# Performance work log

Hardware: AMD Instinct MI355X
Metric: run time of the kernel (lower is better)

## Reference

```python
import jax, jax.numpy as jnp
import numpy as np

EPS = 1e-8  # torch.nn.CosineSimilarity default eps


def setup_inputs() -> dict:
    key = jax.random.key(0)
    ks = jax.random.split(key, 7)
    B, T, D = 2048, 128, 128
    x = jax.random.normal(ks[0], (B, T, D), dtype=jnp.float32)
    def lin(k, fan_out, fan_in):
        kw, kb = jax.random.split(k)
        bound = 1.0 / np.sqrt(fan_in)
        W = jax.random.uniform(kw, (fan_out, fan_in), minval=-bound, maxval=bound, dtype=jnp.float32)
        b = jax.random.uniform(kb, (fan_out,), minval=-bound, maxval=bound, dtype=jnp.float32)
        return W, b
    W1, b1 = lin(ks[1], 96, 128)
    W2, b2 = lin(ks[2], 72, 96)
    W3, b3 = lin(ks[3], 64, 72)
    return {"x": x, "W1": W1, "b1": b1, "W2": W2, "b2": b2, "W3": W3, "b3": b3}


def reference(x, W1, b1, W2, b2, W3, b3):
    # Batched 3-layer MLP (equivalent to the per-slice Python loop).
    h = jax.nn.relu(jnp.einsum('btd,od->bto', x, W1) + b1)
    h = jax.nn.relu(jnp.einsum('bth,oh->bto', h, W2) + b2)
    f = jnp.einsum('bth,oh->bto', h, W3) + b3          # [B, T, 64]
    f = f.reshape(-1, f.shape[-1])                      # [N, 64], N = B*T
    n = jnp.maximum(jnp.linalg.norm(f, axis=-1, keepdims=True), EPS)
    u = f / n                                           # row-normalized feats
    # sum_{i<j} u_i . u_j = (||sum_i u_i||^2 - sum_i ||u_i||^2) / 2
    s = u.sum(axis=0)                                   # [64]
    pair_sum = 0.5 * (jnp.dot(s, s) - jnp.sum(u * u))
    return pair_sum / f.shape[0]
```

## Files before the change

### kernel.cpp

```cpp
#include <hip/hip_runtime.h>

typedef float  f32x4  __attribute__((ext_vector_type(4)));
typedef short  s16x8  __attribute__((ext_vector_type(8)));
typedef short  s16x4  __attribute__((ext_vector_type(4)));

#define NROWS (2048 * 128)
#define PASSES 8
#define HS 104
#define EPSF 1e-8f

union Frag { s16x8 v; unsigned short u[8]; };

__device__ __forceinline__ unsigned short f2bf(float f) {
    unsigned int u = __float_as_uint(f);
    u += 0x7fffu + ((u >> 16) & 1u);
    return (unsigned short)(u >> 16);
}

__global__ void repack(const float* __restrict__ W1, const float* __restrict__ b1,
                       const float* __restrict__ W2, const float* __restrict__ b2,
                       const float* __restrict__ W3, const float* __restrict__ b3,
                       unsigned short* __restrict__ w1f, unsigned short* __restrict__ w2f,
                       unsigned short* __restrict__ w3f,
                       float* __restrict__ b1p, float* __restrict__ b2p,
                       float* __restrict__ b3p)
{
    const int b = blockIdx.x;
    const int l = threadIdx.x;
    const int g = l >> 4, sl = l & 15;

    if (b < 24) {
        const int nt = b >> 2, ks = b & 3;
        const int o = nt * 16 + sl, kb = ks * 32 + g * 8;
        s16x8 v;
#pragma unroll
        for (int j = 0; j < 8; ++j) v[j] = (short)f2bf(W1[o * 128 + kb + j]);
        *(s16x8*)&w1f[b * 512 + l * 8] = v;
    } else if (b < 39) {
        const int f = b - 24, nt = f / 3, ks = f % 3;
        const int o = nt * 16 + sl, kb = ks * 32 + g * 8;
        s16x8 v;
#pragma unroll
        for (int j = 0; j < 8; ++j)
            v[j] = (short)((o < 72) ? f2bf(W2[o * 96 + kb + j]) : 0);
        *(s16x8*)&w2f[f * 512 + l * 8] = v;
    } else if (b < 51) {
        const int f = b - 39, nt = f / 3, ks = f % 3;
        const int o = nt * 16 + sl, kb = ks * 32 + g * 8;
        s16x8 v;
#pragma unroll
        for (int j = 0; j < 8; ++j)
            v[j] = (short)((kb + j < 72) ? f2bf(W3[o * 72 + kb + j]) : 0);
        *(s16x8*)&w3f[f * 512 + l * 8] = v;
    } else {
        for (int i = l; i < 240; i += 64) {
            if (i < 96)       b1p[i] = b1[i];
            else if (i < 176) { int o = i - 96; b2p[o] = (o < 72) ? b2[o] : 0.f; }
            else              b3p[i - 176] = b3[i - 176];
        }
    }
}

__global__ __launch_bounds__(256, 1)
void mlp_main(const float* __restrict__ x,
              const f32x4* __restrict__ w1src,
              const unsigned short* __restrict__ w2f,
              const unsigned short* __restrict__ w3f,
              float* __restrict__ acc )
{
    __shared__ __align__(16) unsigned char  wb[25536];
    __shared__ __align__(16) float          xbuf[4][2048];
    __shared__ __align__(16) unsigned short act[4][16][HS];
    __shared__ float sred[4][64];
    __shared__ float uured[4];

    const unsigned short* w1L = (const unsigned short*)wb;
    const float* b1L = (const float*)(wb + 24576);
    const float* b2L = b1L + 96;
    const float* b3L = b1L + 176;

    const int tid  = threadIdx.x;
    const int lane = tid & 63;
    const int wv   = tid >> 6;
    const int g    = lane >> 4;
    const int sl   = lane & 15;
    const int g4   = g * 4;
    const int wave_gid = blockIdx.x * 4 + wv;

    auto stage = [&](int p) {
        const char* tb = (const char*)x
                       + ((size_t)wave_gid * 128 + (size_t)p * 16) * 512;
        float* dst = &xbuf[wv][0];
#pragma unroll
        for (int c = 0; c < 8; ++c) {
            const unsigned off = (unsigned)(c * 1024 + lane * 16);
            const unsigned so  = off ^ (((off >> 9) & 7u) << 4);
            __builtin_amdgcn_global_load_lds(
                (const __attribute__((address_space(1))) void*)(tb + so),
                (__attribute__((address_space(3))) void*)(dst + c * 256),
                16, 0, 0);
        }
    };

    stage(0);

    for (int i = tid; i < 1596; i += 256)
        ((f32x4*)wb)[i] = w1src[i];

    Frag W2r[5][3], W3r[4][3];
#pragma unroll
    for (int nt = 0; nt < 5; ++nt)
#pragma unroll
        for (int ks = 0; ks < 3; ++ks)
            W2r[nt][ks].v = *(const s16x8*)&w2f[(nt * 3 + ks) * 512 + lane * 8];
#pragma unroll
    for (int nt = 0; nt < 4; ++nt)
#pragma unroll
        for (int ks = 0; ks < 3; ++ks)
            W3r[nt][ks].v = *(const s16x8*)&w3f[(nt * 3 + ks) * 512 + lane * 8];

    __syncthreads();

    float uu_part = 0.f;
    float s_part[4][4];
#pragma unroll
    for (int nt = 0; nt < 4; ++nt)
#pragma unroll
        for (int r = 0; r < 4; ++r) s_part[nt][r] = 0.f;

#pragma unroll 1
    for (int p = 0; p < PASSES; ++p) {
        asm volatile("s_waitcnt vmcnt(0)" ::: "memory");
        __builtin_amdgcn_sched_barrier(0);

        const char* xb = (const char*)&xbuf[wv][0];
        const unsigned sw = (unsigned)((sl & 7) << 4);
        f32x4 t[8];
#pragma unroll
        for (int ks = 0; ks < 4; ++ks)
#pragma unroll
            for (int h = 0; h < 2; ++h)
                t[ks * 2 + h] = *(const f32x4*)(
                    xb + sl * 512 + ks * 128 + (((unsigned)(g * 32 + h * 16)) ^ sw));
        Frag X1[4];
#pragma unroll
        for (int ks = 0; ks < 4; ++ks)
#pragma unroll
            for (int j = 0; j < 4; ++j) {
                X1[ks].u[j]     = f2bf(t[ks * 2 + 0][j]);
                X1[ks].u[4 + j] = f2bf(t[ks * 2 + 1][j]);
            }

        __builtin_amdgcn_sched_barrier(0);
        if (p + 1 < PASSES) stage(p + 1);

        f32x4 D1[6];
#pragma unroll
        for (int nt = 0; nt < 6; ++nt)
            D1[nt] = *(const f32x4*)&b1L[nt * 16 + g4];
#pragma unroll
        for (int ks = 0; ks < 4; ++ks)
#pragma unroll
            for (int nt = 0; nt < 6; ++nt) {
                const s16x8 Wf = *(const s16x8*)&w1L[(nt * 4 + ks) * 512 + lane * 8];
                D1[nt] = __builtin_amdgcn_mfma_f32_16x16x32_bf16(Wf, X1[ks].v, D1[nt], 0, 0, 0);
            }
#pragma unroll
        for (int nt = 0; nt < 6; ++nt) {
            s16x4 q;
#pragma unroll
            for (int j = 0; j < 4; ++j) q[j] = (short)f2bf(fmaxf(D1[nt][j], 0.f));
            *(s16x4*)&act[wv][sl][nt * 16 + g4] = q;
        }

        Frag A2[3];
#pragma unroll
        for (int ks = 0; ks < 3; ++ks)
            A2[ks].v = *(const s16x8*)&act[wv][sl][ks * 32 + g * 8];

        {
            const s16x4 z = (s16x4){0, 0, 0, 0};
            *(s16x4*)&act[wv][sl][80 + g4] = z;
        }

        f32x4 D2[5];
#pragma unroll
        for (int nt = 0; nt < 5; ++nt)
            D2[nt] = *(const f32x4*)&b2L[nt * 16 + g4];
#pragma unroll
        for (int ks = 0; ks < 3; ++ks)
#pragma unroll
            for (int nt = 0; nt < 5; ++nt)
                D2[nt] = __builtin_amdgcn_mfma_f32_16x16x32_bf16(W2r[nt][ks].v, A2[ks].v, D2[nt], 0, 0, 0);
#pragma unroll
        for (int nt = 0; nt < 5; ++nt) {
            s16x4 q;
#pragma unroll
            for (int j = 0; j < 4; ++j) q[j] = (short)f2bf(fmaxf(D2[nt][j], 0.f));
            *(s16x4*)&act[wv][sl][nt * 16 + g4] = q;
        }

        Frag A3[3];
#pragma unroll
        for (int ks = 0; ks < 3; ++ks)
            A3[ks].v = *(const s16x8*)&act[wv][sl][ks * 32 + g * 8];

        f32x4 D3[4];
#pragma unroll
        for (int nt = 0; nt < 4; ++nt)
            D3[nt] = *(const f32x4*)&b3L[nt * 16 + g4];
#pragma unroll
        for (int ks = 0; ks < 3; ++ks)
#pragma unroll
            for (int nt = 0; nt < 4; ++nt)
                D3[nt] = __builtin_amdgcn_mfma_f32_16x16x32_bf16(W3r[nt][ks].v, A3[ks].v, D3[nt], 0, 0, 0);

        float ff = 0.f;
#pragma unroll
        for (int nt = 0; nt < 4; ++nt)
#pragma unroll
            for (int r = 0; r < 4; ++r)
                ff = fmaf(D3[nt][r], D3[nt][r], ff);
        ff += __shfl_xor(ff, 16, 64);
        ff += __shfl_xor(ff, 32, 64);
        const float inv = 1.f / fmaxf(sqrtf(ff), EPSF);
        uu_part = fmaf(ff * inv, inv, uu_part);
#pragma unroll
        for (int nt = 0; nt < 4; ++nt)
#pragma unroll
            for (int r = 0; r < 4; ++r)
                s_part[nt][r] = fmaf(D3[nt][r], inv, s_part[nt][r]);
    }

#pragma unroll
    for (int nt = 0; nt < 4; ++nt)
#pragma unroll
        for (int r = 0; r < 4; ++r) {
            s_part[nt][r] += __shfl_xor(s_part[nt][r], 1, 64);
            s_part[nt][r] += __shfl_xor(s_part[nt][r], 2, 64);
            s_part[nt][r] += __shfl_xor(s_part[nt][r], 4, 64);
            s_part[nt][r] += __shfl_xor(s_part[nt][r], 8, 64);
        }
#pragma unroll
    for (int off = 1; off < 64; off <<= 1)
        uu_part += __shfl_xor(uu_part, off, 64);

    if (sl == 0) {
#pragma unroll
        for (int nt = 0; nt < 4; ++nt) {
            f32x4 v = {s_part[nt][0], s_part[nt][1], s_part[nt][2], s_part[nt][3]};
            *(f32x4*)&sred[wv][nt * 16 + g4] = v;
        }
    }
    if (lane == 0) uured[wv] = uu_part * 0.25f;
    __syncthreads();

    if (tid < 64) {
        const float t2 = sred[0][tid] + sred[1][tid] + sred[2][tid] + sred[3][tid];
        atomicAdd(&acc[tid], t2);
    }
    if (tid == 0)
        atomicAdd(&acc[64], uured[0] + uured[1] + uured[2] + uured[3]);
}

__global__ void finalize_k(const float* __restrict__ acc, float* __restrict__ out)
{
    float s = acc[threadIdx.x];
    float d = s * s;
#pragma unroll
    for (int off = 32; off > 0; off >>= 1)
        d += __shfl_xor(d, off, 64);
    if (threadIdx.x == 0)
        out[0] = 0.5f * (d - acc[64]) / (float)NROWS;
}

extern "C" void kernel_launch(void* const* d_in, const int* in_sizes, int n_in,
                              void* d_out, int out_size, void* d_ws, size_t ws_size,
                              hipStream_t stream)
{
    const float* x  = (const float*)d_in[0];
    const float* W1 = (const float*)d_in[1];
    const float* b1 = (const float*)d_in[2];
    const float* W2 = (const float*)d_in[3];
    const float* b2 = (const float*)d_in[4];
    const float* W3 = (const float*)d_in[5];
    const float* b3 = (const float*)d_in[6];

    char* ws = (char*)d_ws;
    float*          acc = (float*)ws;
    unsigned short* w1f = (unsigned short*)(ws + 1024);
    float*          b1p = (float*)(ws + 25600);
    float*          b2p = (float*)(ws + 25984);
    float*          b3p = (float*)(ws + 26304);
    unsigned short* w2f = (unsigned short*)(ws + 26560);
    unsigned short* w3f = (unsigned short*)(ws + 41920);

    hipMemsetAsync(acc, 0, 1024, stream);
    repack<<<52, 64, 0, stream>>>(W1, b1, W2, b2, W3, b3, w1f, w2f, w3f, b1p, b2p, b3p);
    mlp_main<<<NROWS / (4 * PASSES * 16), 256, 0, stream>>>(
        x, (const f32x4*)(ws + 1024), w2f, w3f, acc);
    finalize_k<<<1, 64, 0, stream>>>(acc, (float*)d_out);
}
```

Before: 53.18 us.

## Fuse weight repack and finalize into single main kernel with last-block reduction

```diff
diff --git a/kernel.cpp b/kernel.cpp
--- a/kernel.cpp
+++ b/kernel.cpp
@@ -8,6 +8,7 @@
 #define PASSES 8
 #define HS 104
 #define EPSF 1e-8f
+#define GRID (NROWS / (4 * PASSES * 16))
 
 union Frag { s16x8 v; unsigned short u[8]; };
 
@@ -17,64 +18,24 @@
     return (unsigned short)(u >> 16);
 }
 
-__global__ void repack(const float* __restrict__ W1, const float* __restrict__ b1,
-                       const float* __restrict__ W2, const float* __restrict__ b2,
-                       const float* __restrict__ W3, const float* __restrict__ b3,
-                       unsigned short* __restrict__ w1f, unsigned short* __restrict__ w2f,
-                       unsigned short* __restrict__ w3f,
-                       float* __restrict__ b1p, float* __restrict__ b2p,
-                       float* __restrict__ b3p)
-{
-    const int b = blockIdx.x;
-    const int l = threadIdx.x;
-    const int g = l >> 4, sl = l & 15;
-
-    if (b < 24) {
-        const int nt = b >> 2, ks = b & 3;
-        const int o = nt * 16 + sl, kb = ks * 32 + g * 8;
-        s16x8 v;
-#pragma unroll
-        for (int j = 0; j < 8; ++j) v[j] = (short)f2bf(W1[o * 128 + kb + j]);
-        *(s16x8*)&w1f[b * 512 + l * 8] = v;
-    } else if (b < 39) {
-        const int f = b - 24, nt = f / 3, ks = f % 3;
-        const int o = nt * 16 + sl, kb = ks * 32 + g * 8;
-        s16x8 v;
-#pragma unroll
-        for (int j = 0; j < 8; ++j)
-            v[j] = (short)((o < 72) ? f2bf(W2[o * 96 + kb + j]) : 0);
-        *(s16x8*)&w2f[f * 512 + l * 8] = v;
-    } else if (b < 51) {
-        const int f = b - 39, nt = f / 3, ks = f % 3;
-        const int o = nt * 16 + sl, kb = ks * 32 + g * 8;
-        s16x8 v;
-#pragma unroll
-        for (int j = 0; j < 8; ++j)
-            v[j] = (short)((kb + j < 72) ? f2bf(W3[o * 72 + kb + j]) : 0);
-        *(s16x8*)&w3f[f * 512 + l * 8] = v;
-    } else {
-        for (int i = l; i < 240; i += 64) {
-            if (i < 96)       b1p[i] = b1[i];
-            else if (i < 176) { int o = i - 96; b2p[o] = (o < 72) ? b2[o] : 0.f; }
-            else              b3p[i - 176] = b3[i - 176];
-        }
-    }
-}
-
 __global__ __launch_bounds__(256, 1)
-void mlp_main(const float* __restrict__ x,
-              const f32x4* __restrict__ w1src,
-              const unsigned short* __restrict__ w2f,
-              const unsigned short* __restrict__ w3f,
-              float* __restrict__ acc )
+void mlp_fused(const float* __restrict__ x,
+               const float* __restrict__ W1, const float* __restrict__ b1,
+               const float* __restrict__ W2, const float* __restrict__ b2,
+               const float* __restrict__ W3, const float* __restrict__ b3,
+               float* __restrict__ acc,
+               float* __restrict__ out)
 {
     __shared__ __align__(16) unsigned char  wb[25536];
     __shared__ __align__(16) float          xbuf[4][2048];
     __shared__ __align__(16) unsigned short act[4][16][HS];
     __shared__ float sred[4][64];
     __shared__ float uured[4];
+    __shared__ unsigned last_flag;
 
     const unsigned short* w1L = (const unsigned short*)wb;
+    unsigned short* w1Lw = (unsigned short*)wb;
+    float* wbias = (float*)(wb + 24576);
     const float* b1L = (const float*)(wb + 24576);
     const float* b2L = b1L + 96;
     const float* b3L = b1L + 176;
@@ -104,20 +65,62 @@
 
     stage(0);
 
-    for (int i = tid; i < 1596; i += 256)
-        ((f32x4*)wb)[i] = w1src[i];
+#pragma unroll
+    for (int it = 0; it < 6; ++it) {
+        const int i = it * 256 + tid;
+        const int f = i >> 6, l = i & 63;
+        const int o  = ((f >> 2) * 16) + (l & 15);
+        const int kb = ((f & 3) * 32) + ((l >> 4) * 8);
+        const f32x4 u0 = *(const f32x4*)(W1 + o * 128 + kb);
+        const f32x4 u1 = *(const f32x4*)(W1 + o * 128 + kb + 4);
+        s16x8 v;
+#pragma unroll
+        for (int j = 0; j < 4; ++j) { v[j] = (short)f2bf(u0[j]); v[4 + j] = (short)f2bf(u1[j]); }
+        *(s16x8*)&w1Lw[f * 512 + l * 8] = v;
+    }
+    if (tid < 240) {
+        float bv;
+        if (tid < 96)       bv = b1[tid];
+        else if (tid < 176) { const int o = tid - 96; bv = (o < 72) ? b2[o] : 0.f; }
+        else                bv = b3[tid - 176];
+        wbias[tid] = bv;
+    }
 
     Frag W2r[5][3], W3r[4][3];
 #pragma unroll
     for (int nt = 0; nt < 5; ++nt)
 #pragma unroll
-        for (int ks = 0; ks < 3; ++ks)
-            W2r[nt][ks].v = *(const s16x8*)&w2f[(nt * 3 + ks) * 512 + lane * 8];
+        for (int ks = 0; ks < 3; ++ks) {
+            const int o = nt * 16 + sl, kb = ks * 32 + g * 8;
+            if (o < 72) {
+                const f32x4 u0 = *(const f32x4*)(W2 + o * 96 + kb);
+                const f32x4 u1 = *(const f32x4*)(W2 + o * 96 + kb + 4);
+#pragma unroll
+                for (int j = 0; j < 4; ++j) {
+                    W2r[nt][ks].u[j]     = f2bf(u0[j]);
+                    W2r[nt][ks].u[4 + j] = f2bf(u1[j]);
+                }
+            } else {
+                W2r[nt][ks].v = (s16x8){0, 0, 0, 0, 0, 0, 0, 0};
+            }
+        }
 #pragma unroll
     for (int nt = 0; nt < 4; ++nt)
 #pragma unroll
-        for (int ks = 0; ks < 3; ++ks)
-            W3r[nt][ks].v = *(const s16x8*)&w3f[(nt * 3 + ks) * 512 + lane * 8];
+        for (int ks = 0; ks < 3; ++ks) {
+            const int o = nt * 16 + sl, kb = ks * 32 + g * 8;
+            if (kb < 72) {
+                const f32x4 u0 = *(const f32x4*)(W3 + o * 72 + kb);
+                const f32x4 u1 = *(const f32x4*)(W3 + o * 72 + kb + 4);
+#pragma unroll
+                for (int j = 0; j < 4; ++j) {
+                    W3r[nt][ks].u[j]     = f2bf(u0[j]);
+                    W3r[nt][ks].u[4 + j] = f2bf(u1[j]);
+                }
+            } else {
+                W3r[nt][ks].v = (s16x8){0, 0, 0, 0, 0, 0, 0, 0};
+            }
+        }
 
     __syncthreads();
 
@@ -261,17 +264,26 @@
     }
     if (tid == 0)
         atomicAdd(&acc[64], uured[0] + uured[1] + uured[2] + uured[3]);
-}
-
-__global__ void finalize_k(const float* __restrict__ acc, float* __restrict__ out)
-{
-    float s = acc[threadIdx.x];
-    float d = s * s;
-#pragma unroll
-    for (int off = 32; off > 0; off >>= 1)
-        d += __shfl_xor(d, off, 64);
-    if (threadIdx.x == 0)
-        out[0] = 0.5f * (d - acc[64]) / (float)NROWS;
+
+    __threadfence();
+    __syncthreads();
+    if (tid == 0) {
+        const unsigned prev = atomicAdd((unsigned*)(acc + 65), 1u);
+        last_flag = (prev == (unsigned)(GRID - 1)) ? 1u : 0u;
+    }
+    __syncthreads();
+    if (last_flag && tid < 64) {
+        __threadfence();
+        const float s  = atomicAdd(&acc[tid], 0.f);
+        float d = s * s;
+#pragma unroll
+        for (int off = 32; off > 0; off >>= 1)
+            d += __shfl_xor(d, off, 64);
+        if (tid == 0) {
+            const float uu = atomicAdd(&acc[64], 0.f);
+            out[0] = 0.5f * (d - uu) / (float)NROWS;
+        }
+    }
 }
 
 extern "C" void kernel_launch(void* const* d_in, const int* in_sizes, int n_in,
@@ -286,18 +298,9 @@
     const float* W3 = (const float*)d_in[5];
     const float* b3 = (const float*)d_in[6];
 
-    char* ws = (char*)d_ws;
-    float*          acc = (float*)ws;
-    unsigned short* w1f = (unsigned short*)(ws + 1024);
-    float*          b1p = (float*)(ws + 25600);
-    float*          b2p = (float*)(ws + 25984);
-    float*          b3p = (float*)(ws + 26304);
-    unsigned short* w2f = (unsigned short*)(ws + 26560);
-    unsigned short* w3f = (unsigned short*)(ws + 41920);
-
+    float* acc = (float*)d_ws;
     hipMemsetAsync(acc, 0, 1024, stream);
-    repack<<<52, 64, 0, stream>>>(W1, b1, W2, b2, W3, b3, w1f, w2f, w3f, b1p, b2p, b3p);
-    mlp_main<<<NROWS / (4 * PASSES * 16), 256, 0, stream>>>(
-        x, (const f32x4*)(ws + 1024), w2f, w3f, acc);
-    finalize_k<<<1, 64, 0, stream>>>(acc, (float*)d_out);
+
+    mlp_fused<<<GRID, 256, 0, stream>>>(x, W1, b1, W2, b2, W3, b3,
+                                        acc, (float*)d_out);
 }
```

Result: slower. 90.34 us (+69.9%).
